# Kernel tuning notes

Hardware: AMD Instinct MI355X
Metric: run time of the kernel (lower is better)

## Reference

```python
import jax, jax.numpy as jnp
import numpy as np

D_MODEL = 1024
NUM_HEADS = 16


def setup_inputs() -> dict:
    key = jax.random.key(0)
    ks = jax.random.split(key, 5)
    std = float(np.sqrt(2.0 / (D_MODEL + D_MODEL)))
    def w(k):
        # approximate trunc_normal init with clipped normal (init only; math of fwd unaffected)
        v = jax.random.truncated_normal(k, -3.0, 3.0, (D_MODEL, D_MODEL), jnp.float32) * std
        return v
    x = jax.random.normal(ks[0], (4, 2048, D_MODEL), jnp.float32)
    return {
        "x": x,
        "wq": w(ks[1]),
        "wk": w(ks[2]),
        "wv": w(ks[3]),
        "wo": w(ks[4]),
    }


def reference(x, wq, wk, wv, wo):
    b, s, d = x.shape
    h = NUM_HEADS
    dk = d // h
    # Linear: einsum('o i, ... i -> ... o')
    def proj(w):
        y = jnp.einsum('oi,bsi->bso', w, x)
        return y.reshape(b, s, h, dk).transpose(0, 2, 1, 3)  # b h s dk
    Q, K, V = proj(wq), proj(wk), proj(wv)
    scale = 1.0 / jnp.sqrt(jnp.asarray(dk, x.dtype))
    scores = jnp.einsum('bhqd,bhkd->bhqk', Q, K) * scale
    mask = jnp.tril(jnp.ones((s, s), dtype=bool))
    scores = jnp.where(mask, scores, -jnp.inf)
    attn = jax.nn.softmax(scores, axis=-1)
    out = jnp.einsum('bhqk,bhkd->bhqd', attn, V)
    out = out.transpose(0, 2, 1, 3).reshape(b, s, d)
    return jnp.einsum('oi,bsi->bso', wo, out)
```

## Files before the change

### kernel.cpp

```cpp
#include <hip/hip_runtime.h>
#include <hip/hip_bf16.h>


typedef __bf16 bf16x8 __attribute__((ext_vector_type(8)));
typedef __bf16 bf16x4 __attribute__((ext_vector_type(4)));
typedef float  f32x4  __attribute__((ext_vector_type(4)));
typedef float  f32x16 __attribute__((ext_vector_type(16)));
typedef unsigned int u32x4_t __attribute__((ext_vector_type(4)));

#define GLOBAL_AS __attribute__((address_space(1)))
#define LDS_AS    __attribute__((address_space(3)))

__device__ __forceinline__ void gload16(const void* g, void* l) {
    __builtin_amdgcn_global_load_lds((const GLOBAL_AS void*)g, (LDS_AS void*)l, 16, 0, 0);
}

__device__ __forceinline__ unsigned int cvtpk_bf16(float lo, float hi) {
    unsigned int r;
    asm("v_cvt_pk_bf16_f32 %0, %1, %2" : "=v"(r) : "v"(lo), "v"(hi));
    return r;
}

#define WAITVM8 asm volatile("s_waitcnt vmcnt(8)" ::: "memory")
#define WAITVM0 asm volatile("s_waitcnt vmcnt(0)" ::: "memory")
#define SCHEDB  __builtin_amdgcn_sched_barrier(0)

__global__ __launch_bounds__(256) void cast_kernel(
    const float* __restrict__ x, const float* __restrict__ wq,
    const float* __restrict__ wk, const float* __restrict__ wv,
    const float* __restrict__ wo, __bf16* __restrict__ xb, __bf16* __restrict__ wb) {
    int bid = blockIdx.x;
    const float* src; __bf16* dst; int base;
    if (bid < 4096) {
        src = x; dst = xb; base = bid * 2048;
    } else {
        int r = bid - 4096; int wi = r >> 9;
        src = (wi == 0) ? wq : (wi == 1) ? wk : (wi == 2) ? wv : wo;
        dst = wb + wi * 1048576; base = (r & 511) * 2048;
    }
    int idx = base + threadIdx.x * 8;
    float4 a = *(const float4*)(src + idx);
    float4 b = *(const float4*)(src + idx + 4);
    bf16x8 o;
    o[0] = (__bf16)a.x; o[1] = (__bf16)a.y; o[2] = (__bf16)a.z; o[3] = (__bf16)a.w;
    o[4] = (__bf16)b.x; o[5] = (__bf16)b.y; o[6] = (__bf16)b.z; o[7] = (__bf16)b.w;
    *(bf16x8*)(dst + idx) = o;
}

__global__ __launch_bounds__(256) void gemm_qkv_kernel(
    const __bf16* __restrict__ A, const __bf16* __restrict__ W,
    __bf16* __restrict__ Qb, __bf16* __restrict__ Kb, __bf16* __restrict__ Vt,
    float qscale) {
    __shared__ __align__(16) char lds[65536];
    const int t = threadIdx.x;
    const int wid = t >> 6, lane = t & 63;
    const int g = lane >> 4, m = lane & 15;
    const int wm = wid >> 1, wn = wid & 1;
    const int bid = (blockIdx.x & 7) * 192 + (blockIdx.x >> 3);
    const int mt = bid / 24, nt = bid % 24;
    const int m0 = mt * 128, n0 = nt * 128;
    const bool isV = (n0 >= 2048);

    const __bf16* sA[4]; const __bf16* sB[4]; int dA[4];
#pragma unroll
    for (int i = 0; i < 4; ++i) {
        const int ci = i * 256 + t;
        const int row = ci >> 3;
        const int k8 = (ci & 7) ^ (row & 7);
        sA[i] = A + (size_t)(m0 + row) * 1024 + k8 * 8;
        sB[i] = W + (size_t)(n0 + row) * 1024 + k8 * 8;
        dA[i] = ci * 16;
    }
    auto stage = [&](int kt, char* buf) {
#pragma unroll
        for (int i = 0; i < 4; ++i) gload16(sA[i] + kt * 64, buf + dA[i]);
#pragma unroll
        for (int i = 0; i < 4; ++i) gload16(sB[i] + kt * 64, buf + 16384 + dA[i]);
    };

    const int sw = (m & 7) << 4;
    const int offA = (wm * 64 + m) * 128 + ((g << 4) ^ sw);
    const int offB = (wn * 64 + m) * 128 + ((g << 4) ^ sw);

    stage(0, lds);

    f32x4 acc[4][4] = {};
    for (int kt = 0; kt < 16; ++kt) {
        char* cbuf = lds + (kt & 1) * 32768;
        if (kt < 15) {
            stage(kt + 1, lds + ((kt + 1) & 1) * 32768);
            WAITVM8;
        } else {
            WAITVM0;
        }
        SCHEDB;
        __builtin_amdgcn_s_barrier();
        SCHEDB;
        const char* bA = cbuf;
        const char* bB = cbuf + 16384;
        bf16x8 a0[4], b0[4], a1[4], b1[4];
#pragma unroll
        for (int i = 0; i < 4; ++i) {
            a0[i] = *(const bf16x8*)(bA + (offA + i * 2048));
            b0[i] = *(const bf16x8*)(bB + (offB + i * 2048));
            a1[i] = *(const bf16x8*)(bA + ((offA + i * 2048) ^ 64));
            b1[i] = *(const bf16x8*)(bB + ((offB + i * 2048) ^ 64));
        }
        __builtin_amdgcn_s_setprio(1);
        if (isV) {
#pragma unroll
            for (int mi = 0; mi < 4; ++mi)
#pragma unroll
                for (int ni = 0; ni < 4; ++ni)
                    acc[mi][ni] = __builtin_amdgcn_mfma_f32_16x16x32_bf16(a0[mi], b0[ni], acc[mi][ni], 0, 0, 0);
#pragma unroll
            for (int mi = 0; mi < 4; ++mi)
#pragma unroll
                for (int ni = 0; ni < 4; ++ni)
                    acc[mi][ni] = __builtin_amdgcn_mfma_f32_16x16x32_bf16(a1[mi], b1[ni], acc[mi][ni], 0, 0, 0);
        } else {
#pragma unroll
            for (int mi = 0; mi < 4; ++mi)
#pragma unroll
                for (int ni = 0; ni < 4; ++ni)
                    acc[mi][ni] = __builtin_amdgcn_mfma_f32_16x16x32_bf16(b0[ni], a0[mi], acc[mi][ni], 0, 0, 0);
#pragma unroll
            for (int mi = 0; mi < 4; ++mi)
#pragma unroll
                for (int ni = 0; ni < 4; ++ni)
                    acc[mi][ni] = __builtin_amdgcn_mfma_f32_16x16x32_bf16(b1[ni], a1[mi], acc[mi][ni], 0, 0, 0);
        }
        __builtin_amdgcn_s_setprio(0);
        if (kt < 15) {
            SCHEDB;
            __builtin_amdgcn_s_barrier();
            SCHEDB;
        }
    }

    if (isV) {
        const int bb = m0 >> 11;
        const int sb = (m0 & 2047) + wm * 64 + 4 * g;
        const int hbase = ((n0 - 2048) >> 6) + wn;
#pragma unroll
        for (int mi = 0; mi < 4; ++mi)
#pragma unroll
            for (int ni = 0; ni < 4; ++ni) {
                const int d = ni * 16 + m;
                bf16x4 pk;
                pk[0] = (__bf16)(acc[mi][ni][0]); pk[1] = (__bf16)(acc[mi][ni][1]);
                pk[2] = (__bf16)(acc[mi][ni][2]); pk[3] = (__bf16)(acc[mi][ni][3]);
                *(bf16x4*)(Vt + ((size_t)(bb * 16 + hbase) * 64 + d) * 2048 + sb + mi * 16) = pk;
            }
    } else {
        __bf16* C = (n0 < 1024) ? Qb : Kb;
        const float sc = (n0 < 1024) ? qscale : 1.f;
        const int cb = (n0 & 1023) + wn * 64 + 4 * g;
        const int row = m0 + wm * 64 + m;
#pragma unroll
        for (int mi = 0; mi < 4; ++mi)
#pragma unroll
            for (int ni = 0; ni < 4; ++ni) {
                bf16x4 pk;
                pk[0] = (__bf16)(acc[mi][ni][0] * sc); pk[1] = (__bf16)(acc[mi][ni][1] * sc);
                pk[2] = (__bf16)(acc[mi][ni][2] * sc); pk[3] = (__bf16)(acc[mi][ni][3] * sc);
                *(bf16x4*)(C + (size_t)(row + mi * 16) * 1024 + cb + ni * 16) = pk;
            }
    }
}

__global__ __launch_bounds__(256) void gemm_out_kernel(
    const __bf16* __restrict__ A, const __bf16* __restrict__ W, float* __restrict__ out) {
    __shared__ __align__(16) char lds[65536];
    const int t = threadIdx.x;
    const int wid = t >> 6, lane = t & 63;
    const int g = lane >> 4, m = lane & 15;
    const int wm = wid >> 1, wn = wid & 1;
    const int bid = (blockIdx.x & 7) * 64 + (blockIdx.x >> 3);
    const int mt = bid >> 3, nt = bid & 7;
    const int m0 = mt * 128, n0 = nt * 128;

    const __bf16* sA[4]; const __bf16* sB[4]; int dA[4];
#pragma unroll
    for (int i = 0; i < 4; ++i) {
        const int ci = i * 256 + t;
        const int row = ci >> 3;
        const int k8 = (ci & 7) ^ (row & 7);
        sA[i] = A + (size_t)(m0 + row) * 1024 + k8 * 8;
        sB[i] = W + (size_t)(n0 + row) * 1024 + k8 * 8;
        dA[i] = ci * 16;
    }
    auto stage = [&](int kt, char* buf) {
#pragma unroll
        for (int i = 0; i < 4; ++i) gload16(sA[i] + kt * 64, buf + dA[i]);
#pragma unroll
        for (int i = 0; i < 4; ++i) gload16(sB[i] + kt * 64, buf + 16384 + dA[i]);
    };

    const int sw = (m & 7) << 4;
    const int offA = (wm * 64 + m) * 128 + ((g << 4) ^ sw);
    const int offB = (wn * 64 + m) * 128 + ((g << 4) ^ sw);

    stage(0, lds);

    f32x4 acc[4][4] = {};
    for (int kt = 0; kt < 16; ++kt) {
        char* cbuf = lds + (kt & 1) * 32768;
        if (kt < 15) {
            stage(kt + 1, lds + ((kt + 1) & 1) * 32768);
            WAITVM8;
        } else {
            WAITVM0;
        }
        SCHEDB;
        __builtin_amdgcn_s_barrier();
        SCHEDB;
        const char* bA = cbuf;
        const char* bB = cbuf + 16384;
        bf16x8 a0[4], b0[4], a1[4], b1[4];
#pragma unroll
        for (int i = 0; i < 4; ++i) {
            a0[i] = *(const bf16x8*)(bA + (offA + i * 2048));
            b0[i] = *(const bf16x8*)(bB + (offB + i * 2048));
            a1[i] = *(const bf16x8*)(bA + ((offA + i * 2048) ^ 64));
            b1[i] = *(const bf16x8*)(bB + ((offB + i * 2048) ^ 64));
        }
        __builtin_amdgcn_s_setprio(1);
#pragma unroll
        for (int mi = 0; mi < 4; ++mi)
#pragma unroll
            for (int ni = 0; ni < 4; ++ni)
                acc[mi][ni] = __builtin_amdgcn_mfma_f32_16x16x32_bf16(b0[ni], a0[mi], acc[mi][ni], 0, 0, 0);
#pragma unroll
        for (int mi = 0; mi < 4; ++mi)
#pragma unroll
            for (int ni = 0; ni < 4; ++ni)
                acc[mi][ni] = __builtin_amdgcn_mfma_f32_16x16x32_bf16(b1[ni], a1[mi], acc[mi][ni], 0, 0, 0);
        __builtin_amdgcn_s_setprio(0);
        if (kt < 15) {
            SCHEDB;
            __builtin_amdgcn_s_barrier();
            SCHEDB;
        }
    }

    const int row = m0 + wm * 64 + m;
    const int col = n0 + wn * 64 + 4 * g;
#pragma unroll
    for (int mi = 0; mi < 4; ++mi)
#pragma unroll
        for (int ni = 0; ni < 4; ++ni)
            *(f32x4*)(out + (size_t)(row + mi * 16) * 1024 + col + ni * 16) = acc[mi][ni];
}

__global__ __launch_bounds__(128) void attn_kernel(
    const __bf16* __restrict__ Qb, const __bf16* __restrict__ Kb,
    const __bf16* __restrict__ Vt, __bf16* __restrict__ Ob) {
    __shared__ __align__(16) char lds[32768];
    const int t = threadIdx.x;
    const int w = t >> 6, lane = t & 63;
    const int l31 = lane & 31, hi = lane >> 5;
    const int x = blockIdx.x;
    const int p = x >> 3;
    const int strip = 31 - (p >> 3);
    const int bh = (x & 7) | ((p & 7) << 3);
    const size_t sbase = (size_t)(bh >> 4) * 2048;
    const int hoff = (bh & 15) * 64;

    const char* Kbase = (const char*)Kb + (sbase * 1024 + hoff) * 2;
    const char* Vbase = (const char*)Vt + (size_t)bh * 262144;
    const int srow = lane >> 3;
    const int scol = ((lane & 7) ^ srow) << 4;
    const int sw = (l31 & 7) << 4;
    int colx[4];
#pragma unroll
    for (int i = 0; i < 4; ++i) colx[i] = (32 * i + 16 * hi) ^ sw;

    auto stage = [&](int kv0, char* lK) {
        char* lV = lK + 8192;
#pragma unroll
        for (int i = 0; i < 4; ++i) {
            const int chunk = i * 2 + w;
            const int row = chunk * 8 + srow;
            gload16(Kbase + (size_t)(kv0 + row) * 2048 + scol, lK + chunk * 1024);
            gload16(Vbase + (size_t)row * 4096 + (size_t)kv0 * 2 + scol, lV + chunk * 1024);
        }
    };

    const int q0w = strip * 64 + w * 32;
    const int q = q0w + l31;
    const int nstream = strip + 1;

    const __bf16* qrow = Qb + (sbase + q0w + l31) * 1024 + hoff + 8 * hi;
    bf16x8 qf[4];
#pragma unroll
    for (int cq = 0; cq < 4; ++cq) qf[cq] = *(const bf16x8*)(qrow + 16 * cq);

    f32x16 o0 = {}, o1 = {};
    float mrun = -__builtin_inff(), lrun = 0.f;

    stage(0, lds);

    for (int tt = 0; tt < nstream; ++tt) {
        const int cur = tt & 1;
        char* lcur = lds + cur * 16384;
        __builtin_amdgcn_s_barrier();
        if (tt + 1 < nstream) {
            stage((tt + 1) * 64, lds + (cur ^ 1) * 16384);
            WAITVM8;
        } else {
            WAITVM0;
        }
        __builtin_amdgcn_s_barrier();
        __builtin_amdgcn_sched_barrier(0);

        const int kv0 = tt * 64;
        const char* lK = lcur;
        const char* lV = lcur + 8192;

        f32x16 s0 = {}, s1 = {};
        __builtin_amdgcn_s_setprio(1);
#pragma unroll
        for (int cc = 0; cc < 4; ++cc) {
            bf16x8 k0 = *(const bf16x8*)(lK + l31 * 128 + colx[cc]);
            bf16x8 k1 = *(const bf16x8*)(lK + (l31 + 32) * 128 + colx[cc]);
            s0 = __builtin_amdgcn_mfma_f32_32x32x16_bf16(k0, qf[cc], s0, 0, 0, 0);
            s1 = __builtin_amdgcn_mfma_f32_32x32x16_bf16(k1, qf[cc], s1, 0, 0, 0);
        }
        __builtin_amdgcn_s_setprio(0);

        float pp[32];
#pragma unroll
        for (int rr = 0; rr < 16; ++rr) { pp[rr] = s0[rr]; pp[16 + rr] = s1[rr]; }
        if (tt == strip) {
#pragma unroll
            for (int rr = 0; rr < 16; ++rr) {
                const int kvl = (rr & 3) + 8 * (rr >> 2) + 4 * hi;
                if (kv0 + kvl > q)      pp[rr]      = -__builtin_inff();
                if (kv0 + 32 + kvl > q) pp[16 + rr] = -__builtin_inff();
            }
        }
        float m8[8];
#pragma unroll
        for (int i = 0; i < 8; ++i)
            m8[i] = fmaxf(fmaxf(pp[4 * i], pp[4 * i + 1]), fmaxf(pp[4 * i + 2], pp[4 * i + 3]));
        float tmax = fmaxf(fmaxf(fmaxf(m8[0], m8[1]), fmaxf(m8[2], m8[3])),
                           fmaxf(fmaxf(m8[4], m8[5]), fmaxf(m8[6], m8[7])));
        const bool skip = __all(tmax <= mrun + 8.f);
        if (!skip) {
            float tq = fmaxf(tmax, __shfl_xor(tmax, 32));
            float mnew = fmaxf(mrun, tq);
            float al = __builtin_amdgcn_exp2f(mrun - mnew);
            lrun *= al;
#pragma unroll
            for (int rr = 0; rr < 16; ++rr) { o0[rr] *= al; o1[rr] *= al; }
            mrun = mnew;
        }
#pragma unroll
        for (int rr = 0; rr < 32; ++rr) pp[rr] = __builtin_amdgcn_exp2f(pp[rr] - mrun);
        float s8[8];
#pragma unroll
        for (int i = 0; i < 8; ++i)
            s8[i] = (pp[4 * i] + pp[4 * i + 1]) + (pp[4 * i + 2] + pp[4 * i + 3]);
        float rsum = ((s8[0] + s8[1]) + (s8[2] + s8[3])) + ((s8[4] + s8[5]) + (s8[6] + s8[7]));
        rsum += __shfl_xor(rsum, 32);
        lrun += rsum;

        __builtin_amdgcn_s_setprio(1);
#pragma unroll
        for (int cc = 0; cc < 4; ++cc) {
            const int pb = cc * 8;
            unsigned int A0 = cvtpk_bf16(pp[pb + 0], pp[pb + 1]);
            unsigned int A1 = cvtpk_bf16(pp[pb + 2], pp[pb + 3]);
            unsigned int B0 = cvtpk_bf16(pp[pb + 4], pp[pb + 5]);
            unsigned int B1 = cvtpk_bf16(pp[pb + 6], pp[pb + 7]);
            asm("v_permlane32_swap_b32 %0, %1" : "+v"(A0), "+v"(B0));
            asm("v_permlane32_swap_b32 %0, %1" : "+v"(A1), "+v"(B1));
            u32x4_t wvv; wvv[0] = A0; wvv[1] = A1; wvv[2] = B0; wvv[3] = B1;
            bf16x8 pa = __builtin_bit_cast(bf16x8, wvv);
            const int vcol = (32 * cc + 16 * hi) ^ sw;
            bf16x8 v0 = *(const bf16x8*)(lV + l31 * 128 + vcol);
            bf16x8 v1 = *(const bf16x8*)(lV + (l31 + 32) * 128 + vcol);
            o0 = __builtin_amdgcn_mfma_f32_32x32x16_bf16(v0, pa, o0, 0, 0, 0);
            o1 = __builtin_amdgcn_mfma_f32_32x32x16_bf16(v1, pa, o1, 0, 0, 0);
        }
        __builtin_amdgcn_s_setprio(0);
    }

    const float inv = 1.f / lrun;
    __bf16* orow = Ob + (sbase + q0w + l31) * 1024 + hoff;
#pragma unroll
    for (int rq = 0; rq < 4; ++rq) {
        bf16x4 e0, e1;
#pragma unroll
        for (int jj = 0; jj < 4; ++jj) {
            e0[jj] = (__bf16)(o0[rq * 4 + jj] * inv);
            e1[jj] = (__bf16)(o1[rq * 4 + jj] * inv);
        }
        *(bf16x4*)(orow + 4 * hi + 8 * rq) = e0;
        *(bf16x4*)(orow + 32 + 4 * hi + 8 * rq) = e1;
    }
}

extern "C" void kernel_launch(void* const* d_in, const int* in_sizes, int n_in,
                              void* d_out, int out_size, void* d_ws, size_t ws_size,
                              hipStream_t stream) {
    const float* x  = (const float*)d_in[0];
    const float* wq = (const float*)d_in[1];
    const float* wk = (const float*)d_in[2];
    const float* wv = (const float*)d_in[3];
    const float* wo = (const float*)d_in[4];

    char* ws = (char*)d_ws;
    __bf16* xb = (__bf16*)(ws);
    __bf16* wb = (__bf16*)(ws + 16777216);
    __bf16* Qb = (__bf16*)(ws + 25165824);
    __bf16* Kb = (__bf16*)(ws + 41943040);
    __bf16* Vt = (__bf16*)(ws + 58720256);
    __bf16* Ob = (__bf16*)(ws + 75497472);

    const float qscale = 0.18033688011112043f;

    cast_kernel<<<6144, 256, 0, stream>>>(x, wq, wk, wv, wo, xb, wb);
    gemm_qkv_kernel<<<1536, 256, 0, stream>>>(xb, wb, Qb, Kb, Vt, qscale);
    attn_kernel<<<2048, 128, 0, stream>>>(Qb, Kb, Vt, Ob);
    gemm_out_kernel<<<512, 256, 0, stream>>>(Ob, wb + 3145728, (float*)d_out);
}
```

Baseline: 181.0 us.

## Load K/V fragments directly into registers instead of staging through LDS

The attention kernel drops its double-buffered LDS staging of K and V tiles and the barriers around it. Each wave now loads its own K and V MFMA operands straight from global memory into registers, prefetching the next tile's K right after the QK MFMAs and the next V right after the PV MFMAs. This removes LDS traffic and block-wide synchronisation. In exchange, the two waves each fetch the same K/V data (no sharing), register pressure rises, and global latency is only hidden by the softmax work between loads.

```diff
diff --git a/kernel.cpp b/kernel.cpp
--- a/kernel.cpp
+++ b/kernel.cpp
@@ -256,7 +256,6 @@
 __global__ __launch_bounds__(128) void attn_kernel(
     const __bf16* __restrict__ Qb, const __bf16* __restrict__ Kb,
     const __bf16* __restrict__ Vt, __bf16* __restrict__ Ob) {
-    __shared__ __align__(16) char lds[32768];
     const int t = threadIdx.x;
     const int w = t >> 6, lane = t & 63;
     const int l31 = lane & 31, hi = lane >> 5;
@@ -269,28 +268,16 @@
 
     const char* Kbase = (const char*)Kb + (sbase * 1024 + hoff) * 2;
     const char* Vbase = (const char*)Vt + (size_t)bh * 262144;
-    const int srow = lane >> 3;
-    const int scol = ((lane & 7) ^ srow) << 4;
-    const int sw = (l31 & 7) << 4;
-    int colx[4];
-#pragma unroll
-    for (int i = 0; i < 4; ++i) colx[i] = (32 * i + 16 * hi) ^ sw;
-
-    auto stage = [&](int kv0, char* lK) {
-        char* lV = lK + 8192;
-#pragma unroll
-        for (int i = 0; i < 4; ++i) {
-            const int chunk = i * 2 + w;
-            const int row = chunk * 8 + srow;
-            gload16(Kbase + (size_t)(kv0 + row) * 2048 + scol, lK + chunk * 1024);
-            gload16(Vbase + (size_t)row * 4096 + (size_t)kv0 * 2 + scol, lV + chunk * 1024);
-        }
-    };
 
     const int q0w = strip * 64 + w * 32;
     const int q = q0w + l31;
     const int nstream = strip + 1;
 
+    const char* Krow0 = Kbase + (size_t)l31 * 2048 + 16 * hi;
+    const char* Krow1 = Kbase + (size_t)(l31 + 32) * 2048 + 16 * hi;
+    const char* Vrow0 = Vbase + (size_t)l31 * 4096 + 16 * hi;
+    const char* Vrow1 = Vbase + (size_t)(l31 + 32) * 4096 + 16 * hi;
+
     const __bf16* qrow = Qb + (sbase + q0w + l31) * 1024 + hoff + 8 * hi;
     bf16x8 qf[4];
 #pragma unroll
@@ -299,35 +286,36 @@
     f32x16 o0 = {}, o1 = {};
     float mrun = -__builtin_inff(), lrun = 0.f;
 
-    stage(0, lds);
+    bf16x8 k0[4], k1[4], v0[4], v1[4];
+#pragma unroll
+    for (int cc = 0; cc < 4; ++cc) {
+        k0[cc] = *(const bf16x8*)(Krow0 + 32 * cc);
+        k1[cc] = *(const bf16x8*)(Krow1 + 32 * cc);
+        v0[cc] = *(const bf16x8*)(Vrow0 + 32 * cc);
+        v1[cc] = *(const bf16x8*)(Vrow1 + 32 * cc);
+    }
 
     for (int tt = 0; tt < nstream; ++tt) {
-        const int cur = tt & 1;
-        char* lcur = lds + cur * 16384;
-        __builtin_amdgcn_s_barrier();
-        if (tt + 1 < nstream) {
-            stage((tt + 1) * 64, lds + (cur ^ 1) * 16384);
-            WAITVM8;
-        } else {
-            WAITVM0;
-        }
-        __builtin_amdgcn_s_barrier();
-        __builtin_amdgcn_sched_barrier(0);
-
         const int kv0 = tt * 64;
-        const char* lK = lcur;
-        const char* lV = lcur + 8192;
 
         f32x16 s0 = {}, s1 = {};
         __builtin_amdgcn_s_setprio(1);
 #pragma unroll
         for (int cc = 0; cc < 4; ++cc) {
-            bf16x8 k0 = *(const bf16x8*)(lK + l31 * 128 + colx[cc]);
-            bf16x8 k1 = *(const bf16x8*)(lK + (l31 + 32) * 128 + colx[cc]);
-            s0 = __builtin_amdgcn_mfma_f32_32x32x16_bf16(k0, qf[cc], s0, 0, 0, 0);
-            s1 = __builtin_amdgcn_mfma_f32_32x32x16_bf16(k1, qf[cc], s1, 0, 0, 0);
+            s0 = __builtin_amdgcn_mfma_f32_32x32x16_bf16(k0[cc], qf[cc], s0, 0, 0, 0);
+            s1 = __builtin_amdgcn_mfma_f32_32x32x16_bf16(k1[cc], qf[cc], s1, 0, 0, 0);
         }
         __builtin_amdgcn_s_setprio(0);
+        SCHEDB;
+        if (tt + 1 < nstream) {
+            const size_t ko = (size_t)(kv0 + 64) * 2048;
+#pragma unroll
+            for (int cc = 0; cc < 4; ++cc) {
+                k0[cc] = *(const bf16x8*)(Krow0 + ko + 32 * cc);
+                k1[cc] = *(const bf16x8*)(Krow1 + ko + 32 * cc);
+            }
+        }
+        SCHEDB;
 
         float pp[32];
 #pragma unroll
@@ -378,13 +366,20 @@
             asm("v_permlane32_swap_b32 %0, %1" : "+v"(A1), "+v"(B1));
             u32x4_t wvv; wvv[0] = A0; wvv[1] = A1; wvv[2] = B0; wvv[3] = B1;
             bf16x8 pa = __builtin_bit_cast(bf16x8, wvv);
-            const int vcol = (32 * cc + 16 * hi) ^ sw;
-            bf16x8 v0 = *(const bf16x8*)(lV + l31 * 128 + vcol);
-            bf16x8 v1 = *(const bf16x8*)(lV + (l31 + 32) * 128 + vcol);
-            o0 = __builtin_amdgcn_mfma_f32_32x32x16_bf16(v0, pa, o0, 0, 0, 0);
-            o1 = __builtin_amdgcn_mfma_f32_32x32x16_bf16(v1, pa, o1, 0, 0, 0);
+            o0 = __builtin_amdgcn_mfma_f32_32x32x16_bf16(v0[cc], pa, o0, 0, 0, 0);
+            o1 = __builtin_amdgcn_mfma_f32_32x32x16_bf16(v1[cc], pa, o1, 0, 0, 0);
         }
         __builtin_amdgcn_s_setprio(0);
+        SCHEDB;
+        if (tt + 1 < nstream) {
+            const size_t vo = (size_t)(kv0 + 64) * 2;
+#pragma unroll
+            for (int cc = 0; cc < 4; ++cc) {
+                v0[cc] = *(const bf16x8*)(Vrow0 + vo + 32 * cc);
+                v1[cc] = *(const bf16x8*)(Vrow1 + vo + 32 * cc);
+            }
+        }
+        SCHEDB;
     }
 
     const float inv = 1.f / lrun;
```

Result: slower. 240.2 us (+32.7%).
